# Kernel optimization log

Hardware: AMD Instinct MI355X
Metric: run time of the kernel (lower is better)

## Reference

```python
import jax, jax.numpy as jnp
import numpy as np

ALPHA = 0.9   # synaptic decay
BETA = 0.8    # membrane decay
THRESH = 1.0  # snntorch default threshold, reset_mechanism='subtract'
DIMS = [7200, 3600, 1800, 900, 450]
B, T, IN_DIM, K = 128, 16, 14400, 25


def setup_inputs() -> dict:
    key = jax.random.key(0)
    ks = jax.random.split(key, 24)
    inp = {}
    inp["x"] = jax.random.normal(ks[0], (B, T, IN_DIM), jnp.float32)
    prev = IN_DIM
    for i, d in enumerate(DIMS):
        inp[f"w{i}"] = jax.random.normal(ks[1 + i], (d, K), jnp.float32) * (2.0 / K) ** 0.5
        inp[f"b{i}"] = jax.random.normal(ks[7 + i], (d,), jnp.float32) * 0.01
        inp[f"knn{i}"] = jax.random.randint(ks[13 + i], (d, K), 0, prev)
        prev = d
    inp["fc_w"] = jax.random.normal(ks[20], (2, DIMS[-1]), jnp.float32) * 0.05
    inp["fc_b"] = jax.random.normal(ks[21], (2,), jnp.float32) * 0.01
    return inp


def _forward(x, ws, bs, knns, fc_w, fc_b):
    n_layer = len(DIMS)

    def lif(inp, syn, mem):
        # snntorch Synaptic, reset_mechanism='subtract': reset computed from
        # the PREVIOUS membrane potential and detached from the graph.
        reset = jax.lax.stop_gradient((mem > THRESH).astype(inp.dtype))
        syn = ALPHA * syn + inp
        mem = BETA * mem + syn - reset * THRESH
        return syn, mem

    def step(carry, xt):
        syns, mems = carry
        h = xt  # (B, prev_dim)
        new_syns, new_mems = [], []
        for i in range(n_layer):
            g = jnp.take(h, knns[i], axis=1)                 # (B, d_i, K) KNN gather
            pre = jnp.einsum('bdk,dk->bd', g, ws[i]) + bs[i]  # weighted sum over K
            syn, mem = lif(pre, syns[i], mems[i])
            new_syns.append(syn)
            new_mems.append(mem)
            h = mem  # module propagates membrane potential to next layer
        angle = h @ fc_w.T + fc_b  # (B, 2)
        return (tuple(new_syns), tuple(new_mems)), angle

    bsz = x.shape[0]
    syns0 = tuple(jnp.zeros((bsz, d), x.dtype) for d in DIMS)
    mems0 = tuple(jnp.zeros((bsz, d), x.dtype) for d in DIMS)
    _, angles = jax.lax.scan(step, (syns0, mems0), jnp.transpose(x, (1, 0, 2)))
    return angles[-1]  # only the final timestep's angle is returned


def reference(x, w0, w1, w2, w3, w4, b0, b1, b2, b3, b4,
              knn0, knn1, knn2, knn3, knn4, fc_w, fc_b):
    return _forward(x, (w0, w1, w2, w3, w4), (b0, b1, b2, b3, b4),
                    (knn0, knn1, knn2, knn3, knn4), fc_w, fc_b)
```

## Files before the change

kernel.cpp:

```cpp
#include <hip/hip_runtime.h>

#define ALPHA 0.9f
#define BETA  0.8f
#define K     25
#define B     128
#define T     16
#define IN_DIM 14400
#define NSL   8
#define SW    16
#define CF    96
#define NCH   150

using u16 = unsigned short;

static __device__ __forceinline__ u16 f2bf(float f) {
  union { float f; unsigned u; } c; c.f = f;
  const unsigned r = c.u + 0x7FFFu + ((c.u >> 16) & 1u);
  return (u16)(r >> 16);
}
static __device__ __forceinline__ float bf2f(u16 h) {
  union { unsigned u; float f; } c; c.u = ((unsigned)h) << 16;
  return c.f;
}

__global__ __launch_bounds__(256, 4) void transpose_pair_pinned(
    const float* __restrict__ x, u16* __restrict__ xTh, int t0, int slots) {
  __shared__ float lds[CF][33];
  const int e    = blockIdx.x & 7;
  const int slot = blockIdx.x >> 3;
  const int tid  = threadIdx.x;
  const int rid  = tid >> 3;
  const int fq   = tid & 7;
  const int tpar = rid >> 4;
  const int bl   = rid & 15;
  const int b    = e * 16 + bl;

  const int ntiles = 4 * NCH;
  for (int ti = slot; ti < ntiles; ti += slots) {
    const int tp = ti / NCH;
    const int ch = ti - tp * NCH;
    const int i0 = ch * CF;
    const int t  = t0 + tp * 2 + tpar;
    const float* xr = x + ((size_t)b * T + t) * IN_DIM + i0;
#pragma unroll
    for (int pf = 0; pf < CF / 32; ++pf) {
      const float4 v = *(const float4*)&xr[pf * 32 + fq * 4];
      lds[pf * 32 + fq * 4 + 0][rid] = v.x;
      lds[pf * 32 + fq * 4 + 1][rid] = v.y;
      lds[pf * 32 + fq * 4 + 2][rid] = v.z;
      lds[pf * 32 + fq * 4 + 3][rid] = v.w;
    }
    __syncthreads();
#pragma unroll
    for (int wp = 0; wp < CF / 32; ++wp) {
      const int f = wp * 32 + rid;
      ushort4 ov;
      ov.x = f2bf(lds[f][fq * 4 + 0]);
      ov.y = f2bf(lds[f][fq * 4 + 1]);
      ov.z = f2bf(lds[f][fq * 4 + 2]);
      ov.w = f2bf(lds[f][fq * 4 + 3]);
      *(ushort4*)&xTh[(((size_t)tp * NSL + e) * IN_DIM + (i0 + f)) * 32 +
                      fq * 4] = ov;
    }
    __syncthreads();
  }
}

template <int NTP, int NPASS>
__global__ __launch_bounds__(256, 4) void lcn_pair_lds(
    const u16* __restrict__ hsrc, const float* __restrict__ w,
    const float* __restrict__ bias, const int* __restrict__ knn,
    u16* __restrict__ memout, float* __restrict__ state,
    int dim, int dprev, int nblk, int load_state, int save_state) {
  __shared__ int   sidx[32][K];
  __shared__ float swr[32][K];

  const int e    = blockIdx.x & 7;
  const int blk  = blockIdx.x >> 3;
  const int nl   = threadIdx.x >> 3;
  const int l8   = threadIdx.x & 7;
  const int half = l8 >> 2;
  const int bq   = (l8 & 3) * 4;
  const int lofs = half * SW + bq;

#pragma unroll 1
  for (int p = 0; p < NPASS; ++p) {
    const int dbase = (blk + p * nblk) * 32;
    const int dd  = dbase + nl;
    const bool act = dd < dim;
    const int d   = act ? dd : dim - 1;

    __syncthreads();
    for (int i = threadIdx.x; i < 32 * K; i += 256) {
      const int n = i / K, k = i - n * K;
      int dn = dbase + n;
      if (dn >= dim) dn = dim - 1;
      sidx[n][k] = knn[dn * K + k] * 32;
      swr[n][k]  = w[dn * K + k];
    }
    __syncthreads();

    const float bi = bias[d];

    float4 s = make_float4(0.f, 0.f, 0.f, 0.f);
    float4 m = make_float4(0.f, 0.f, 0.f, 0.f);
    if (load_state) {
      const size_t so = ((size_t)e * dim + d) * SW + bq;
      s = *(const float4*)&state[so];
      m = *(const float4*)&state[(size_t)NSL * dim * SW + so];
    }

    for (int tp = 0; tp < NTP; ++tp) {
      const u16* hp = hsrc + ((size_t)tp * NSL + e) * dprev * 32;
      ushort4 ha[9], hb[8];
#pragma unroll
      for (int j = 0; j < 9; ++j)
        ha[j] = *(const ushort4*)&hp[sidx[nl][j] + lofs];
#pragma unroll
      for (int j = 0; j < 8; ++j)
        hb[j] = *(const ushort4*)&hp[sidx[nl][9 + j] + lofs];
      float4 a0 = make_float4(bi, bi, bi, bi);
      float4 a1 = make_float4(0.f, 0.f, 0.f, 0.f);
#pragma unroll
      for (int j = 0; j < 9; ++j) {
        const float wk = swr[nl][j];
        if (j & 1) {
          a1.x = fmaf(wk, bf2f(ha[j].x), a1.x);
          a1.y = fmaf(wk, bf2f(ha[j].y), a1.y);
          a1.z = fmaf(wk, bf2f(ha[j].z), a1.z);
          a1.w = fmaf(wk, bf2f(ha[j].w), a1.w);
        } else {
          a0.x = fmaf(wk, bf2f(ha[j].x), a0.x);
          a0.y = fmaf(wk, bf2f(ha[j].y), a0.y);
          a0.z = fmaf(wk, bf2f(ha[j].z), a0.z);
          a0.w = fmaf(wk, bf2f(ha[j].w), a0.w);
        }
      }
#pragma unroll
      for (int j = 0; j < 8; ++j)
        ha[j] = *(const ushort4*)&hp[sidx[nl][17 + j] + lofs];
#pragma unroll
      for (int j = 0; j < 8; ++j) {
        const float wk = swr[nl][9 + j];
        if (j & 1) {
          a1.x = fmaf(wk, bf2f(hb[j].x), a1.x);
          a1.y = fmaf(wk, bf2f(hb[j].y), a1.y);
          a1.z = fmaf(wk, bf2f(hb[j].z), a1.z);
          a1.w = fmaf(wk, bf2f(hb[j].w), a1.w);
        } else {
          a0.x = fmaf(wk, bf2f(hb[j].x), a0.x);
          a0.y = fmaf(wk, bf2f(hb[j].y), a0.y);
          a0.z = fmaf(wk, bf2f(hb[j].z), a0.z);
          a0.w = fmaf(wk, bf2f(hb[j].w), a0.w);
        }
      }
#pragma unroll
      for (int j = 0; j < 8; ++j) {
        const float wk = swr[nl][17 + j];
        if (j & 1) {
          a1.x = fmaf(wk, bf2f(ha[j].x), a1.x);
          a1.y = fmaf(wk, bf2f(ha[j].y), a1.y);
          a1.z = fmaf(wk, bf2f(ha[j].z), a1.z);
          a1.w = fmaf(wk, bf2f(ha[j].w), a1.w);
        } else {
          a0.x = fmaf(wk, bf2f(ha[j].x), a0.x);
          a0.y = fmaf(wk, bf2f(ha[j].y), a0.y);
          a0.z = fmaf(wk, bf2f(ha[j].z), a0.z);
          a0.w = fmaf(wk, bf2f(ha[j].w), a0.w);
        }
      }
      float4 acc;
      acc.x = a0.x + a1.x;
      acc.y = a0.y + a1.y;
      acc.z = a0.z + a1.z;
      acc.w = a0.w + a1.w;
      float4 oth;
      oth.x = __shfl_xor(acc.x, 4, 64);
      oth.y = __shfl_xor(acc.y, 4, 64);
      oth.z = __shfl_xor(acc.z, 4, 64);
      oth.w = __shfl_xor(acc.w, 4, 64);
      const float4 pre0 = half ? oth : acc;
      const float4 pre1 = half ? acc : oth;
      s.x = ALPHA * s.x + pre0.x;
      s.y = ALPHA * s.y + pre0.y;
      s.z = ALPHA * s.z + pre0.z;
      s.w = ALPHA * s.w + pre0.w;
      float4 meven;
      meven.x = BETA * m.x + s.x - ((m.x > 1.0f) ? 1.0f : 0.0f);
      meven.y = BETA * m.y + s.y - ((m.y > 1.0f) ? 1.0f : 0.0f);
      meven.z = BETA * m.z + s.z - ((m.z > 1.0f) ? 1.0f : 0.0f);
      meven.w = BETA * m.w + s.w - ((m.w > 1.0f) ? 1.0f : 0.0f);
      s.x = ALPHA * s.x + pre1.x;
      s.y = ALPHA * s.y + pre1.y;
      s.z = ALPHA * s.z + pre1.z;
      s.w = ALPHA * s.w + pre1.w;
      m.x = BETA * meven.x + s.x - ((meven.x > 1.0f) ? 1.0f : 0.0f);
      m.y = BETA * meven.y + s.y - ((meven.y > 1.0f) ? 1.0f : 0.0f);
      m.z = BETA * meven.z + s.z - ((meven.z > 1.0f) ? 1.0f : 0.0f);
      m.w = BETA * meven.w + s.w - ((meven.w > 1.0f) ? 1.0f : 0.0f);
      if (act) {
        const float4 wv = half ? m : meven;
        ushort4 ov;
        ov.x = f2bf(wv.x);
        ov.y = f2bf(wv.y);
        ov.z = f2bf(wv.z);
        ov.w = f2bf(wv.w);
        *(ushort4*)&memout[(((size_t)tp * NSL + e) * dim + d) * 32 +
                           half * SW + bq] = ov;
      }
    }

    if (save_state && act && half == 0) {
      const size_t so = ((size_t)e * dim + d) * SW + bq;
      *(float4*)&state[so] = s;
      *(float4*)&state[(size_t)NSL * dim * SW + so] = m;
    }
  }
}

__global__ __launch_bounds__(128) void fc_kernel(
    const u16* __restrict__ mem4, const float* __restrict__ fc_w,
    const float* __restrict__ fc_b, float* __restrict__ out) {
  const int b  = threadIdx.x;
  const int e  = b >> 4;
  const int bl = b & 15;
  float a0 = fc_b[0], a1 = fc_b[1];
  const u16* base = mem4 + ((size_t)7 * NSL + e) * 450 * 32;
  for (int d = 0; d < 450; ++d) {
    const float h = bf2f(base[(size_t)d * 32 + SW + bl]);
    a0 += fc_w[d] * h;
    a1 += fc_w[450 + d] * h;
  }
  out[b * 2 + 0] = a0;
  out[b * 2 + 1] = a1;
}

extern "C" void kernel_launch(void* const* d_in, const int* in_sizes, int n_in,
                              void* d_out, int out_size, void* d_ws,
                              size_t ws_size, hipStream_t stream) {
  (void)in_sizes; (void)n_in; (void)out_size; (void)ws_size;
  const float* x = (const float*)d_in[0];
  const float* w[5];
  const float* bias[5];
  const int* knn[5];
  for (int i = 0; i < 5; ++i) {
    w[i]    = (const float*)d_in[1 + 3 * i];
    bias[i] = (const float*)d_in[2 + 3 * i];
    knn[i]  = (const int*)d_in[3 + 3 * i];
  }
  const float* fc_w = (const float*)d_in[16];
  const float* fc_b = (const float*)d_in[17];
  float* out = (float*)d_out;

  static const int DIMS[5] = {7200, 3600, 1800, 900, 450};

  u16* A  = (u16*)d_ws;
  u16* XB = A + 14745600;
  float* S = (float*)(XB + 14745600);

  u16* mem0 = A;
  u16* mem1 = XB;
  u16* mem2 = A;
  u16* mem3 = XB + 7372800;
  u16* mem4 = A;

  for (int stage = 0; stage < 2; ++stage) {
    const int t0 = stage * 8;
    transpose_pair_pinned<<<128 * NSL, 256, 0, stream>>>(x, XB, t0, 128);
    lcn_pair_lds<4, 2><<<113 * NSL, 256, 0, stream>>>(
        XB, w[0], bias[0], knn[0], mem0 + (size_t)stage * 7372800, S,
        DIMS[0], IN_DIM, 113, stage, stage == 0);
  }

  static const int NBLK[5] = {113, 113, 57, 29, 15};
  const u16* src = mem0;
  u16* dsts[4] = {mem1, mem2, mem3, mem4};
  for (int i = 1; i < 5; ++i) {
    lcn_pair_lds<8, 1><<<NBLK[i] * NSL, 256, 0, stream>>>(
        src, w[i], bias[i], knn[i], dsts[i - 1], nullptr, DIMS[i],
        DIMS[i - 1], NBLK[i], 0, 0);
    src = dsts[i - 1];
  }

  fc_kernel<<<1, 128, 0, stream>>>(mem4, fc_w, fc_b, out);
}
```

Before: 346.9 us.

## Transpose all timesteps at once and run layer 0 in one state-free pass

The two-stage scheme is replaced: all 16 timesteps of the input are transposed to bf16 in one launch, and layer 0 runs once over all 8 time pairs. That removes the synaptic and membrane state save and reload between stages and two kernel launches. Each layer-0 block now handles two neuron sets interleaved inside the time loop, with their index and weight tables loaded into LDS once. The transpose writes time pairs in reverse order so the earliest pairs, which layer 0 reads first, are the most recently written and more likely still in cache. The transposed buffer doubles in size, which needs more workspace and may extend past the old layout.

```diff
diff --git a/kernel.cpp b/kernel.cpp
--- a/kernel.cpp
+++ b/kernel.cpp
@@ -23,8 +23,8 @@
   return c.f;
 }
 
-__global__ __launch_bounds__(256, 4) void transpose_pair_pinned(
-    const float* __restrict__ x, u16* __restrict__ xTh, int t0, int slots) {
+__global__ __launch_bounds__(256, 4) void transpose_full(
+    const float* __restrict__ x, u16* __restrict__ xTh, int slots) {
   __shared__ float lds[CF][33];
   const int e    = blockIdx.x & 7;
   const int slot = blockIdx.x >> 3;
@@ -35,12 +35,12 @@
   const int bl   = rid & 15;
   const int b    = e * 16 + bl;
 
-  const int ntiles = 4 * NCH;
+  const int ntiles = 8 * NCH;
   for (int ti = slot; ti < ntiles; ti += slots) {
-    const int tp = ti / NCH;
-    const int ch = ti - tp * NCH;
+    const int tp = 7 - ti / NCH;
+    const int ch = ti % NCH;
     const int i0 = ch * CF;
-    const int t  = t0 + tp * 2 + tpar;
+    const int t  = tp * 2 + tpar;
     const float* xr = x + ((size_t)b * T + t) * IN_DIM + i0;
 #pragma unroll
     for (int pf = 0; pf < CF / 32; ++pf) {
@@ -66,14 +66,13 @@
   }
 }
 
-template <int NTP, int NPASS>
-__global__ __launch_bounds__(256, 4) void lcn_pair_lds(
+template <int NTP, int NSETS>
+__global__ __launch_bounds__(256, 4) void lcn_ss(
     const u16* __restrict__ hsrc, const float* __restrict__ w,
     const float* __restrict__ bias, const int* __restrict__ knn,
-    u16* __restrict__ memout, float* __restrict__ state,
-    int dim, int dprev, int nblk, int load_state, int save_state) {
-  __shared__ int   sidx[32][K];
-  __shared__ float swr[32][K];
+    u16* __restrict__ memout, int dim, int dprev, int nblk) {
+  __shared__ int   sidx[32 * NSETS][K];
+  __shared__ float swr[32 * NSETS][K];
 
   const int e    = blockIdx.x & 7;
   const int blk  = blockIdx.x >> 3;
@@ -83,47 +82,51 @@
   const int bq   = (l8 & 3) * 4;
   const int lofs = half * SW + bq;
 
-#pragma unroll 1
-  for (int p = 0; p < NPASS; ++p) {
-    const int dbase = (blk + p * nblk) * 32;
-    const int dd  = dbase + nl;
-    const bool act = dd < dim;
-    const int d   = act ? dd : dim - 1;
-
-    __syncthreads();
-    for (int i = threadIdx.x; i < 32 * K; i += 256) {
-      const int n = i / K, k = i - n * K;
-      int dn = dbase + n;
-      if (dn >= dim) dn = dim - 1;
-      sidx[n][k] = knn[dn * K + k] * 32;
-      swr[n][k]  = w[dn * K + k];
-    }
-    __syncthreads();
-
-    const float bi = bias[d];
-
-    float4 s = make_float4(0.f, 0.f, 0.f, 0.f);
-    float4 m = make_float4(0.f, 0.f, 0.f, 0.f);
-    if (load_state) {
-      const size_t so = ((size_t)e * dim + d) * SW + bq;
-      s = *(const float4*)&state[so];
-      m = *(const float4*)&state[(size_t)NSL * dim * SW + so];
-    }
-
-    for (int tp = 0; tp < NTP; ++tp) {
-      const u16* hp = hsrc + ((size_t)tp * NSL + e) * dprev * 32;
+  for (int i = threadIdx.x; i < 32 * NSETS * K; i += 256) {
+    const int n = i / K, k = i - n * K;
+    int dn = (blk + (n >> 5) * nblk) * 32 + (n & 31);
+    if (dn >= dim) dn = dim - 1;
+    sidx[n][k] = knn[dn * K + k] * 32;
+    swr[n][k]  = w[dn * K + k];
+  }
+  __syncthreads();
+
+  int   dset[NSETS];
+  bool  aset[NSETS];
+  float bset[NSETS];
+#pragma unroll
+  for (int q = 0; q < NSETS; ++q) {
+    const int dd = (blk + q * nblk) * 32 + nl;
+    aset[q] = dd < dim;
+    dset[q] = aset[q] ? dd : dim - 1;
+    bset[q] = bias[dset[q]];
+  }
+
+  float4 sv[NSETS], mv[NSETS];
+#pragma unroll
+  for (int q = 0; q < NSETS; ++q) {
+    sv[q] = make_float4(0.f, 0.f, 0.f, 0.f);
+    mv[q] = make_float4(0.f, 0.f, 0.f, 0.f);
+  }
+
+  for (int tp = 0; tp < NTP; ++tp) {
+    const u16* hp = hsrc + ((size_t)tp * NSL + e) * dprev * 32;
+#pragma unroll
+    for (int q = 0; q < NSETS; ++q) {
+      const int nr = q * 32 + nl;
+      const float bi = bset[q];
       ushort4 ha[9], hb[8];
 #pragma unroll
       for (int j = 0; j < 9; ++j)
-        ha[j] = *(const ushort4*)&hp[sidx[nl][j] + lofs];
+        ha[j] = *(const ushort4*)&hp[sidx[nr][j] + lofs];
 #pragma unroll
       for (int j = 0; j < 8; ++j)
-        hb[j] = *(const ushort4*)&hp[sidx[nl][9 + j] + lofs];
+        hb[j] = *(const ushort4*)&hp[sidx[nr][9 + j] + lofs];
       float4 a0 = make_float4(bi, bi, bi, bi);
       float4 a1 = make_float4(0.f, 0.f, 0.f, 0.f);
 #pragma unroll
       for (int j = 0; j < 9; ++j) {
-        const float wk = swr[nl][j];
+        const float wk = swr[nr][j];
         if (j & 1) {
           a1.x = fmaf(wk, bf2f(ha[j].x), a1.x);
           a1.y = fmaf(wk, bf2f(ha[j].y), a1.y);
@@ -138,10 +141,10 @@
       }
 #pragma unroll
       for (int j = 0; j < 8; ++j)
-        ha[j] = *(const ushort4*)&hp[sidx[nl][17 + j] + lofs];
+        ha[j] = *(const ushort4*)&hp[sidx[nr][17 + j] + lofs];
 #pragma unroll
       for (int j = 0; j < 8; ++j) {
-        const float wk = swr[nl][9 + j];
+        const float wk = swr[nr][9 + j];
         if (j & 1) {
           a1.x = fmaf(wk, bf2f(hb[j].x), a1.x);
           a1.y = fmaf(wk, bf2f(hb[j].y), a1.y);
@@ -156,7 +159,7 @@
       }
 #pragma unroll
       for (int j = 0; j < 8; ++j) {
-        const float wk = swr[nl][17 + j];
+        const float wk = swr[nr][17 + j];
         if (j & 1) {
           a1.x = fmaf(wk, bf2f(ha[j].x), a1.x);
           a1.y = fmaf(wk, bf2f(ha[j].y), a1.y);
@@ -181,6 +184,7 @@
       oth.w = __shfl_xor(acc.w, 4, 64);
       const float4 pre0 = half ? oth : acc;
       const float4 pre1 = half ? acc : oth;
+      float4 s = sv[q], m = mv[q];
       s.x = ALPHA * s.x + pre0.x;
       s.y = ALPHA * s.y + pre0.y;
       s.z = ALPHA * s.z + pre0.z;
@@ -198,22 +202,18 @@
       m.y = BETA * meven.y + s.y - ((meven.y > 1.0f) ? 1.0f : 0.0f);
       m.z = BETA * meven.z + s.z - ((meven.z > 1.0f) ? 1.0f : 0.0f);
       m.w = BETA * meven.w + s.w - ((meven.w > 1.0f) ? 1.0f : 0.0f);
-      if (act) {
+      sv[q] = s;
+      mv[q] = m;
+      if (aset[q]) {
         const float4 wv = half ? m : meven;
         ushort4 ov;
         ov.x = f2bf(wv.x);
         ov.y = f2bf(wv.y);
         ov.z = f2bf(wv.z);
         ov.w = f2bf(wv.w);
-        *(ushort4*)&memout[(((size_t)tp * NSL + e) * dim + d) * 32 +
+        *(ushort4*)&memout[(((size_t)tp * NSL + e) * dim + dset[q]) * 32 +
                            half * SW + bq] = ov;
       }
-    }
-
-    if (save_state && act && half == 0) {
-      const size_t so = ((size_t)e * dim + d) * SW + bq;
-      *(float4*)&state[so] = s;
-      *(float4*)&state[(size_t)NSL * dim * SW + so] = m;
     }
   }
 }
@@ -252,11 +252,8 @@
   const float* fc_b = (const float*)d_in[17];
   float* out = (float*)d_out;
 
-  static const int DIMS[5] = {7200, 3600, 1800, 900, 450};
-
   u16* A  = (u16*)d_ws;
   u16* XB = A + 14745600;
-  float* S = (float*)(XB + 14745600);
 
   u16* mem0 = A;
   u16* mem1 = XB;
@@ -264,23 +261,18 @@
   u16* mem3 = XB + 7372800;
   u16* mem4 = A;
 
-  for (int stage = 0; stage < 2; ++stage) {
-    const int t0 = stage * 8;
-    transpose_pair_pinned<<<128 * NSL, 256, 0, stream>>>(x, XB, t0, 128);
-    lcn_pair_lds<4, 2><<<113 * NSL, 256, 0, stream>>>(
-        XB, w[0], bias[0], knn[0], mem0 + (size_t)stage * 7372800, S,
-        DIMS[0], IN_DIM, 113, stage, stage == 0);
-  }
-
-  static const int NBLK[5] = {113, 113, 57, 29, 15};
-  const u16* src = mem0;
-  u16* dsts[4] = {mem1, mem2, mem3, mem4};
-  for (int i = 1; i < 5; ++i) {
-    lcn_pair_lds<8, 1><<<NBLK[i] * NSL, 256, 0, stream>>>(
-        src, w[i], bias[i], knn[i], dsts[i - 1], nullptr, DIMS[i],
-        DIMS[i - 1], NBLK[i], 0, 0);
-    src = dsts[i - 1];
-  }
+  transpose_full<<<128 * NSL, 256, 0, stream>>>(x, XB, 128);
+
+  lcn_ss<8, 2><<<113 * NSL, 256, 0, stream>>>(
+      XB, w[0], bias[0], knn[0], mem0, 7200, IN_DIM, 113);
+  lcn_ss<8, 1><<<113 * NSL, 256, 0, stream>>>(
+      mem0, w[1], bias[1], knn[1], mem1, 3600, 7200, 113);
+  lcn_ss<8, 1><<<57 * NSL, 256, 0, stream>>>(
+      mem1, w[2], bias[2], knn[2], mem2, 1800, 3600, 57);
+  lcn_ss<8, 1><<<29 * NSL, 256, 0, stream>>>(
+      mem2, w[3], bias[3], knn[3], mem3, 900, 1800, 29);
+  lcn_ss<8, 1><<<15 * NSL, 256, 0, stream>>>(
+      mem3, w[4], bias[4], knn[4], mem4, 450, 900, 15);
 
   fc_kernel<<<1, 128, 0, stream>>>(mem4, fc_w, fc_b, out);
 }
```

New measurement: 845.4 us. 2.44x slower.
